# Optimization experiments

Hardware: AMD Instinct MI355X
Metric: run time of the kernel (lower is better)

The kernel has to match this reference:

```python
import jax, jax.numpy as jnp
import numpy as np

N, DEG, FIN, FOUT, K = 50000, 16, 32, 64, 3
E = N * DEG


def setup_inputs() -> dict:
    key = jax.random.key(0)
    ks = jax.random.split(key, 10)
    rng = np.random.default_rng(0)
    # unique edges sorted row-major (src*N+dst), ring guarantees deg_in/out>0
    ring = np.arange(N, dtype=np.int64) * N + (np.arange(N, dtype=np.int64) + 1) % N
    cand = np.unique(rng.integers(0, N * N, size=3 * E, dtype=np.int64))
    cand = np.setdiff1d(cand, ring, assume_unique=True)[: E - N]
    codes = np.sort(np.concatenate([cand, ring]))
    assert codes.shape[0] == E
    edge_index = jnp.asarray(np.stack([codes // N, codes % N]).astype(np.int32))
    X = jax.random.normal(ks[0], (N, FIN), jnp.float32)
    edge_weight = jax.random.uniform(ks[1], (E,), jnp.float32, 0.5, 1.5)
    cin = FIN + FOUT
    xav = float(np.sqrt(6.0 / (cin + FOUT)))
    def w(k):
        return jax.random.uniform(k, (2, K, cin, FOUT), jnp.float32, -xav, xav)
    return {
        'X': X, 'edge_index': edge_index, 'edge_weight': edge_weight,
        'Wz': w(ks[2]), 'bz': jnp.zeros((FOUT,), jnp.float32),
        'Wr': w(ks[3]), 'br': jnp.zeros((FOUT,), jnp.float32),
        'Wh': w(ks[4]), 'bh': jnp.zeros((FOUT,), jnp.float32),
    }


def _dconv(X, src, dst, rev_src, rev_dst, norm_out, norm_in, W, b):
    n = X.shape[0]
    def prop(x, s, d, nrm):  # out[d] += nrm * x[s]
        return jax.ops.segment_sum(nrm[:, None] * x[s], d, num_segments=n)
    H = X @ W[0, 0] + X @ W[1, 0]
    if W.shape[1] > 1:
        Tx1o = prop(X, src, dst, norm_out)
        Tx1i = prop(X, rev_src, rev_dst, norm_in)
        H = H + Tx1o @ W[0, 1] + Tx1i @ W[1, 1]
        for k in range(2, W.shape[1]):
            Tx1o = 2.0 * prop(Tx1o, src, dst, norm_out) - X
            Tx1i = 2.0 * prop(Tx1i, rev_src, rev_dst, norm_in) - X
            H = H + Tx1o @ W[0, k] + Tx1i @ W[1, k]
    return H + b


def reference(X, edge_index, edge_weight, Wz, bz, Wr, br, Wh, bh):
    n = X.shape[0]
    src, dst = edge_index[0], edge_index[1]
    deg_out = jax.ops.segment_sum(edge_weight, src, num_segments=n)
    deg_in = jax.ops.segment_sum(edge_weight, dst, num_segments=n)
    # faithful to original: both norms indexed by row (source)
    norm_out = 1.0 / deg_out[src]
    norm_in = 1.0 / deg_in[src]
    # reverse edges in dense_to_sparse(adj.T) order: sorted by (dst, src)
    order = jnp.argsort(dst.astype(jnp.int64) * n + src.astype(jnp.int64))
    rev_src, rev_dst = dst[order], src[order]
    H = jnp.zeros((n, Wz.shape[-1]), X.dtype)
    dc = lambda inp, W, b: _dconv(inp, src, dst, rev_src, rev_dst, norm_out, norm_in, W, b)
    Z = jax.nn.sigmoid(dc(jnp.concatenate([X, H], axis=1), Wz, bz))
    R = jax.nn.sigmoid(dc(jnp.concatenate([X, H], axis=1), Wr, br))
    H_tilde = jnp.tanh(dc(jnp.concatenate([X, H * R], axis=1), Wh, bh))
    return Z * H + (1.0 - Z) * H_tilde
```

## Files before the change

kernel.cpp:

```cpp
#include <hip/hip_runtime.h>
#include <hip/hip_fp16.h>
#include <cmath>

#define NN 50000
#define NE 800000
#define PADF 96
#define NBIN 391
#define NBLK 391
#define FCAP 3072
#define DST_HI 42949
#define SRC_CUT 33648

__device__ __forceinline__ unsigned short f2h(float f) {
  __half h = __float2half_rn(f);
  return *reinterpret_cast<unsigned short*>(&h);
}

typedef _Float16 half4 __attribute__((ext_vector_type(4)));
typedef float f32x4 __attribute__((ext_vector_type(4)));

__global__ __launch_bounds__(256) void k_aux(const float* __restrict__ X, const int* __restrict__ src,
                                             const int* __restrict__ dst, const float* __restrict__ ew,
                                             int* __restrict__ H,
                                             int* __restrict__ rptr, float* __restrict__ dout,
                                             const float* __restrict__ Wz, const float* __restrict__ Wh,
                                             unsigned short* __restrict__ WT, unsigned short* __restrict__ Xh,
                                             int* __restrict__ s0g) {
  __shared__ int hh[NBIN];
  __shared__ int s0l;
  int bid = blockIdx.x;
  int t = threadIdx.x;
  if (bid >= 667) {
    int h = bid - 667;
    hh[t] = 0;
    if (t + 256 < NBIN) hh[t + 256] = 0;
    if (t == 0) s0l = 0;
    __syncthreads();
    int my = 0;
#pragma unroll
    for (int r = 0; r < 8; ++r) {
      int e = h * 2048 + r * 256 + t;
      if (e < NE) {
        int d = dst[e];
        atomicAdd(&hh[d >> 7], 1);
        my += (d < DST_HI) ? 1 : 0;
        my += (d == DST_HI && src[e] < SRC_CUT) ? 1 : 0;
      }
    }
    atomicAdd(&s0l, my);
    __syncthreads();
    H[t * NBLK + h] = hh[t];
    if (t + 256 < NBIN) H[(t + 256) * NBLK + h] = hh[t + 256];
    if (t == 0) atomicAdd(s0g, s0l);
  } else if (bid < 196) {
    int i = bid * 256 + t;
    if (i >= NN) return;
    int lo = 0, hi = NE;
    while (lo < hi) { int m = (lo + hi) >> 1; if (src[m] < i) lo = m + 1; else hi = m; }
    int lo2 = lo, hi2 = NE;
    while (lo2 < hi2) { int m = (lo2 + hi2) >> 1; if (src[m] < i + 1) lo2 = m + 1; else hi2 = m; }
    rptr[i] = lo;
    if (i == NN - 1) rptr[NN] = lo2;
    float a = 0.f;
    for (int p = lo; p < lo2; ++p) a += ew[p];
    dout[i] = a;
  } else if (bid < 276) {
    int idx = (bid - 196) * 256 + t;
    int kk = idx >> 7, f = idx & 127;
    int blk = kk >> 5, c = kk & 31;
    const float* W = (f < 64) ? Wz : Wh;
    int fl = f & 63;
    float v;
    if (blk == 0)      v = W[c * 64 + fl] + W[18432 + c * 64 + fl];
    else if (blk == 1) v = W[6144 + c * 64 + fl];
    else if (blk == 2) v = W[18432 + 6144 + c * 64 + fl];
    else if (blk == 3) v = W[2 * 6144 + c * 64 + fl];
    else               v = W[18432 + 2 * 6144 + c * 64 + fl];
    WT[f * 160 + kk] = f2h(v);
  } else {
    int tt = (bid - 276) * 256 + t;
    int base = tt * 16;
    if (base >= NN * 32) return;
#pragma unroll
    for (int q = 0; q < 2; ++q) {
      const float4 a = *(const float4*)&X[base + q * 8];
      const float4 b = *(const float4*)&X[base + q * 8 + 4];
      ushort4 o1 = make_ushort4(f2h(a.x), f2h(a.y), f2h(a.z), f2h(a.w));
      ushort4 o2 = make_ushort4(f2h(b.x), f2h(b.y), f2h(b.z), f2h(b.w));
      *(ushort4*)&Xh[base + q * 8] = o1;
      *(ushort4*)&Xh[base + q * 8 + 4] = o2;
    }
  }
}

__global__ __launch_bounds__(512) void k_scanrow(int* __restrict__ H, int* __restrict__ rowtot) {
  __shared__ int tmp[512];
  int row = blockIdx.x;
  int t = threadIdx.x;
  int v = (t < NBLK) ? H[row * NBLK + t] : 0;
  tmp[t] = v;
  __syncthreads();
  for (int off = 1; off < 512; off <<= 1) {
    int u = (t >= (unsigned)off) ? tmp[t - off] : 0;
    __syncthreads();
    tmp[t] += u;
    __syncthreads();
  }
  if (t < NBLK) H[row * NBLK + t] = tmp[t] - v;
  if (t == 511) rowtot[row] = tmp[511];
}

__global__ __launch_bounds__(512) void k_part(const int* __restrict__ src, const int* __restrict__ dst,
                                              const int* __restrict__ P, const int* __restrict__ rowtot,
                                              unsigned long long* __restrict__ cmp64) {
  __shared__ int loc[NBIN];
  __shared__ int rs[512];
  __shared__ int rbase[NBIN];
  int h = blockIdx.x;
  int t = threadIdx.x;
  int v = (t < NBIN) ? rowtot[t] : 0;
  rs[t] = v;
  if (t < NBIN) loc[t] = 0;
  __syncthreads();
  for (int off = 1; off < 512; off <<= 1) {
    int u = (t >= (unsigned)off) ? rs[t - off] : 0;
    __syncthreads();
    rs[t] += u;
    __syncthreads();
  }
  if (t < NBIN) rbase[t] = rs[t] - v;
  __syncthreads();
#pragma unroll
  for (int r = 0; r < 4; ++r) {
    int e = h * 2048 + r * 512 + t;
    if (e < NE) {
      int d = dst[e];
      int bin = d >> 7;
      int rk = atomicAdd(&loc[bin], 1);
      int pos = rbase[bin] + P[bin * NBLK + h] + rk;
      cmp64[pos] = ((unsigned long long)(d & 127) << 48) |
                   ((unsigned long long)src[e] << 24) | (unsigned long long)e;
    }
  }
}

__global__ __launch_bounds__(512) void k_fine(const int* __restrict__ rowtot, const float* __restrict__ ew,
                                              const unsigned long long* __restrict__ cmp64,
                                              int2* __restrict__ cmp, int* __restrict__ sp,
                                              float* __restrict__ din) {
  __shared__ unsigned long long a1[FCAP], a2[FCAP];
  __shared__ int fh[128], fcnt[128], fo[129];
  __shared__ int bs[2];
  int cb = blockIdx.x;
  int t = threadIdx.x;
  if (t < 64) {
    int s = 0;
    for (int i = t; i < cb; i += 64) s += rowtot[i];
    s += __shfl_xor(s, 32, 64); s += __shfl_xor(s, 16, 64); s += __shfl_xor(s, 8, 64);
    s += __shfl_xor(s, 4, 64);  s += __shfl_xor(s, 2, 64);  s += __shfl_xor(s, 1, 64);
    if (t == 0) { bs[0] = s; bs[1] = s + rowtot[cb]; }
  }
  if (t < 128) { fh[t] = 0; fcnt[t] = 0; }
  __syncthreads();
  int base = bs[0];
  int m = bs[1] - base;
  if (m > FCAP) m = FCAP;
  for (int i = t; i < m; i += 512) {
    unsigned long long it = cmp64[base + i];
    a1[i] = it;
    atomicAdd(&fh[(int)(it >> 48)], 1);
  }
  __syncthreads();
  if (t < 64) {
    int v0 = fh[t * 2], v1 = fh[t * 2 + 1];
    int pair = v0 + v1;
    int run = pair;
    for (int off = 1; off < 64; off <<= 1) {
      int v = __shfl_up(run, off, 64);
      if (t >= off) run += v;
    }
    int excl = run - pair;
    fo[t * 2] = excl; fo[t * 2 + 1] = excl + v0;
    if (t == 63) fo[128] = excl + pair;
  }
  __syncthreads();
  for (int i = t; i < m; i += 512) {
    unsigned long long it = a1[i];
    int b = (int)(it >> 48);
    int p2 = fo[b] + atomicAdd(&fcnt[b], 1);
    a2[p2] = it;
  }
  if (t < 128) {
    int d = cb * 128 + t;
    if (d <= NN) sp[d] = base + fo[t];
  }
  __syncthreads();
  const int wv0 = t >> 6, lane = t & 63;
  for (int seg = wv0; seg < 128; seg += 8) {
    int d = cb * 128 + seg;
    if (d >= NN) break;
    int f0 = fo[seg], f1 = fo[seg + 1];
    int n = f1 - f0;
    int b0g = base + f0;
    if (n > 64) {
      if (lane == 0) {
        unsigned long long arr[PADF];
        int nn = n > PADF ? PADF : n;
        for (int i = 0; i < nn; ++i) arr[i] = a2[f0 + i];
        for (int i = 1; i < nn; ++i) {
          unsigned long long v = arr[i]; int j = i - 1;
          while (j >= 0 && arr[j] > v) { arr[j + 1] = arr[j]; --j; }
          arr[j + 1] = v;
        }
        float s = 0.f;
        for (int i = 0; i < nn; ++i) {
          unsigned long long it = arr[i];
          int e = (int)(it & 0xFFFFFF);
          int sc = (int)((it >> 24) & 0xFFFF);
          s += ew[e];
          cmp[b0g + i] = make_int2(e, (int)(((unsigned)d << 16) | (unsigned)sc));
        }
        din[d] = s;
      }
      continue;
    }
    unsigned long long k = ~0ULL;
    if (lane < n) k = a2[f0 + lane];
    if (n > 1) {
#pragma unroll
      for (int kk = 2; kk <= 64; kk <<= 1) {
#pragma unroll
        for (int j = kk >> 1; j > 0; j >>= 1) {
          unsigned long long o = __shfl_xor(k, j, 64);
          bool lower = (lane & j) == 0;
          bool asc = (lane & kk) == 0;
          bool keepmin = (lower == asc);
          if (keepmin ? (o < k) : (o > k)) k = o;
        }
      }
    }
    float wsum = 0.f;
    if (lane < n) {
      int e = (int)(k & 0xFFFFFF);
      int sc = (int)((k >> 24) & 0xFFFF);
      wsum = ew[e];
      cmp[b0g + lane] = make_int2(e, (int)(((unsigned)d << 16) | (unsigned)sc));
    }
    wsum += __shfl_xor(wsum, 32, 64); wsum += __shfl_xor(wsum, 16, 64);
    wsum += __shfl_xor(wsum, 8, 64);  wsum += __shfl_xor(wsum, 4, 64);
    wsum += __shfl_xor(wsum, 2, 64);  wsum += __shfl_xor(wsum, 1, 64);
    if (lane == 0) din[d] = wsum;
  }
}

__global__ __launch_bounds__(256) void k_emit(const int2* __restrict__ cmp, const int* __restrict__ rawsrc,
                                              const float* __restrict__ dout, const float* __restrict__ din,
                                              const int* __restrict__ s0g,
                                              int2* __restrict__ cnf, int2* __restrict__ cnr) {
  int i = blockIdx.x * 256 + threadIdx.x;
  if (i >= NE) return;
  int2 c = cmp[i];
  int e = c.x;
  unsigned y = (unsigned)c.y;
  int d = (int)(y >> 16), sc = (int)(y & 0xFFFF);
  cnf[i] = make_int2(sc, __float_as_int(1.0f / dout[sc]));
  int j = i - s0g[0]; if (j < 0) j += NE;
  cnr[e] = make_int2(d, __float_as_int(1.0f / din[rawsrc[j]]));
}

__global__ __launch_bounds__(256) void k_prop2(const unsigned short* __restrict__ inA, const int* __restrict__ rpA,
                                               const int2* __restrict__ cnA, unsigned short* __restrict__ outAh,
                                               const unsigned short* __restrict__ inB, const int* __restrict__ rpB,
                                               const int2* __restrict__ cnB, unsigned short* __restrict__ outBh,
                                               const float* __restrict__ sub, float mul) {
  int t = blockIdx.x * 256 + threadIdx.x;
  const int half = NN * 8;
  const unsigned short* in; const int* rp; const int2* cn; unsigned short* outh;
  if (t < half) { in = inA; rp = rpA; cn = cnA; outh = outAh; }
  else          { in = inB; rp = rpB; cn = cnB; outh = outBh; t -= half; }
  int r = t >> 3;
  if (r >= NN) return;
  int lane8 = t & 7;
  int c4 = lane8 * 4;
  int b = rp[r], e2 = rp[r + 1];
  float a0[4] = {0.f, 0.f, 0.f, 0.f}, a1[4] = {0.f, 0.f, 0.f, 0.f};
  int p = b;
#define GATH(cc, ww) { \
    uint2 bv = *(const uint2*)&in[(cc) * 32 + c4]; \
    float2 f01 = __half22float2(*(const __half2*)&bv.x); \
    float2 f23 = __half22float2(*(const __half2*)&bv.y); \
    float* a = (jj & 1) ? a1 : a0; \
    a[0] += (ww) * f01.x; a[1] += (ww) * f01.y; \
    a[2] += (ww) * f23.x; a[3] += (ww) * f23.y; }
  for (; p + 16 <= e2; p += 16) {
    int2 u = cn[p + lane8];
    int2 v = cn[p + 8 + lane8];
#pragma unroll
    for (int jj = 0; jj < 8; ++jj) {
      int col = __shfl(u.x, jj, 8);
      float w = __int_as_float(__shfl(u.y, jj, 8));
      GATH(col, w)
    }
#pragma unroll
    for (int jj = 0; jj < 8; ++jj) {
      int col = __shfl(v.x, jj, 8);
      float w = __int_as_float(__shfl(v.y, jj, 8));
      GATH(col, w)
    }
  }
  for (; p + 8 <= e2; p += 8) {
    int2 u = cn[p + lane8];
#pragma unroll
    for (int jj = 0; jj < 8; ++jj) {
      int col = __shfl(u.x, jj, 8);
      float w = __int_as_float(__shfl(u.y, jj, 8));
      GATH(col, w)
    }
  }
  for (int jj = 0; p < e2; ++p) {
    int2 c1 = cn[p];
    float w = __int_as_float(c1.y);
    GATH(c1.x, w)
  }
#undef GATH
  float ax = a0[0] + a1[0], ay = a0[1] + a1[1], az = a0[2] + a1[2], aw = a0[3] + a1[3];
  float4 o;
  if (sub) {
    const float4 s = *(const float4*)&sub[r * 32 + c4];
    o.x = mul * ax - s.x; o.y = mul * ay - s.y; o.z = mul * az - s.z; o.w = mul * aw - s.w;
  } else {
    o.x = ax; o.y = ay; o.z = az; o.w = aw;
  }
  ushort4 oh = make_ushort4(f2h(o.x), f2h(o.y), f2h(o.z), f2h(o.w));
  *(ushort4*)&outh[r * 32 + c4] = oh;
}

__global__ __launch_bounds__(256) void k_gemm(const unsigned short* __restrict__ Xh,
                                              const unsigned short* __restrict__ T1oh,
                                              const unsigned short* __restrict__ T1ih,
                                              const unsigned short* __restrict__ T2oh,
                                              const unsigned short* __restrict__ T2ih,
                                              const unsigned short* __restrict__ WT,
                                              const float* __restrict__ bz, const float* __restrict__ bh,
                                              float* __restrict__ out) {
  __shared__ unsigned short wlds[128 * 168];
  const int tid = threadIdx.x;
  for (int i = tid; i < 128 * 20; i += 256) {
    int n = i / 20, o = i % 20;
    *(uint4*)&wlds[n * 168 + o * 8] = *(const uint4*)&WT[n * 160 + o * 8];
  }
  __syncthreads();
  const int l = tid & 63, wid = tid >> 6;
  const int m0 = wid * 16;
  const int rb = blockIdx.x * 64;
  int grow = rb + m0 + (l & 15); if (grow >= NN) grow = NN - 1;
  const int kg = (l >> 4) * 4;
  f32x4 acc[8];
#pragma unroll
  for (int t = 0; t < 8; ++t) acc[t] = (f32x4){0.f, 0.f, 0.f, 0.f};
  const unsigned short* srcs[5] = {Xh, T1oh, T1ih, T2oh, T2ih};
#pragma unroll
  for (int s = 0; s < 5; ++s) {
    const unsigned short* A = srcs[s];
#pragma unroll
    for (int h2 = 0; h2 < 2; ++h2) {
      const int kk = h2 * 16;
      half4 af = *(const half4*)&A[grow * 32 + kk + kg];
      const int kglob = s * 32 + kk + kg;
#pragma unroll
      for (int t = 0; t < 8; ++t) {
        half4 bf = *(const half4*)&wlds[(t * 16 + (l & 15)) * 168 + kglob];
        acc[t] = __builtin_amdgcn_mfma_f32_16x16x16f16(af, bf, acc[t], 0, 0, 0);
      }
    }
  }
  const int c = l & 15;
#pragma unroll
  for (int t = 0; t < 4; ++t) {
    int col = t * 16 + c;
    float bzv = bz[col], bhv = bh[col];
#pragma unroll
    for (int i = 0; i < 4; ++i) {
      int r = rb + m0 + (l >> 4) * 4 + i;
      if (r < NN) {
        float z = 1.f / (1.f + expf(-(acc[t][i] + bzv)));
        float hv = tanhf(acc[t + 4][i] + bhv);
        out[r * 64 + col] = (1.f - z) * hv;
      }
    }
  }
}

extern "C" void kernel_launch(void* const* d_in, const int* in_sizes, int n_in,
                              void* d_out, int out_size, void* d_ws, size_t ws_size,
                              hipStream_t stream) {
  const float* X  = (const float*)d_in[0];
  const int*   ei = (const int*)d_in[1];
  const float* ew = (const float*)d_in[2];
  const float* Wz = (const float*)d_in[3];
  const float* bz = (const float*)d_in[4];
  const float* Wh = (const float*)d_in[7];
  const float* bh = (const float*)d_in[8];
  float* out = (float*)d_out;
  const int* src = ei;
  const int* dst = ei + NE;

  char* p = (char*)d_ws;
  auto alloc = [&](size_t bytes) -> char* {
    char* r = p;
    p += (bytes + 255) & ~(size_t)255;
    return r;
  };
  unsigned short* Xh   = (unsigned short*)alloc((size_t)NN * 32 * 2);
  unsigned short* T1oh = (unsigned short*)alloc((size_t)NN * 32 * 2);
  unsigned short* T1ih = (unsigned short*)alloc((size_t)NN * 32 * 2);
  unsigned short* T2oh = (unsigned short*)alloc((size_t)NN * 32 * 2);
  unsigned short* T2ih = (unsigned short*)alloc((size_t)NN * 32 * 2);
  unsigned long long* cmp64 = (unsigned long long*)alloc((size_t)NE * 8);
  int2*  cmp     = (int2*)alloc((size_t)NE * 8);
  int2*  cnf     = (int2*)alloc((size_t)NE * 8);
  int2*  cnr     = (int2*)alloc((size_t)NE * 8);
  int*   H       = (int*)alloc((size_t)NBIN * NBLK * 4);
  int*   rowtot  = (int*)alloc(NBIN * 4);
  int*   sp      = (int*)alloc((NN + 1) * 4);
  int*   rptr    = (int*)alloc((NN + 1) * 4);
  float* dout    = (float*)alloc(NN * 4);
  float* din     = (float*)alloc(NN * 4);
  unsigned short* WT = (unsigned short*)alloc(128 * 160 * 2);
  int*   s0g     = (int*)alloc(256);

  hipMemsetAsync(s0g, 0, 4, stream);
  k_aux<<<1058, 256, 0, stream>>>(X, src, dst, ew, H, rptr, dout, Wz, Wh, WT, Xh, s0g);
  k_scanrow<<<NBIN, 512, 0, stream>>>(H, rowtot);
  k_part<<<NBLK, 512, 0, stream>>>(src, dst, H, rowtot, cmp64);
  k_fine<<<NBIN, 512, 0, stream>>>(rowtot, ew, cmp64, cmp, sp, din);
  k_emit<<<3125, 256, 0, stream>>>(cmp, src, dout, din, s0g, cnf, cnr);

  k_prop2<<<3125, 256, 0, stream>>>(Xh, sp, cnf, T1oh,
                                    Xh, rptr, cnr, T1ih, nullptr, 1.f);
  k_prop2<<<3125, 256, 0, stream>>>(T1oh, sp, cnf, T2oh,
                                    T1ih, rptr, cnr, T2ih, X, 2.f);

  k_gemm<<<782, 256, 0, stream>>>(Xh, T1oh, T1ih, T2oh, T2ih, WT, bz, bh, out);
}
```

Baseline: 259.4 us.

## Move per-destination bitonic sort from k_fine into fused sort+emit kernel

The per-destination segment sort, previously done by 8 waves per block inside k_fine, moves into a new wave-per-node kernel (k_sortw). That kernel sorts each segment and writes the normalized forward and reverse edge arrays directly, replacing k_emit. k_fine now writes unsorted compacted entries and computes in-degree sums with 4 lanes per node. The aim is more parallelism for the sort across 12500 blocks. The cost is an extra read of cmp and scattered per-edge writes into cnr.

```diff
diff --git a/kernel.cpp b/kernel.cpp
--- a/kernel.cpp
+++ b/kernel.cpp
@@ -195,77 +195,80 @@
     if (d <= NN) sp[d] = base + fo[t];
   }
   __syncthreads();
-  const int wv0 = t >> 6, lane = t & 63;
-  for (int seg = wv0; seg < 128; seg += 8) {
-    int d = cb * 128 + seg;
-    if (d >= NN) break;
-    int f0 = fo[seg], f1 = fo[seg + 1];
-    int n = f1 - f0;
-    int b0g = base + f0;
-    if (n > 64) {
-      if (lane == 0) {
-        unsigned long long arr[PADF];
-        int nn = n > PADF ? PADF : n;
-        for (int i = 0; i < nn; ++i) arr[i] = a2[f0 + i];
-        for (int i = 1; i < nn; ++i) {
-          unsigned long long v = arr[i]; int j = i - 1;
-          while (j >= 0 && arr[j] > v) { arr[j + 1] = arr[j]; --j; }
-          arr[j + 1] = v;
-        }
-        float s = 0.f;
-        for (int i = 0; i < nn; ++i) {
-          unsigned long long it = arr[i];
-          int e = (int)(it & 0xFFFFFF);
-          int sc = (int)((it >> 24) & 0xFFFF);
-          s += ew[e];
-          cmp[b0g + i] = make_int2(e, (int)(((unsigned)d << 16) | (unsigned)sc));
-        }
-        din[d] = s;
-      }
-      continue;
-    }
-    unsigned long long k = ~0ULL;
-    if (lane < n) k = a2[f0 + lane];
-    if (n > 1) {
-#pragma unroll
-      for (int kk = 2; kk <= 64; kk <<= 1) {
-#pragma unroll
-        for (int j = kk >> 1; j > 0; j >>= 1) {
-          unsigned long long o = __shfl_xor(k, j, 64);
-          bool lower = (lane & j) == 0;
-          bool asc = (lane & kk) == 0;
-          bool keepmin = (lower == asc);
-          if (keepmin ? (o < k) : (o > k)) k = o;
-        }
-      }
-    }
-    float wsum = 0.f;
-    if (lane < n) {
-      int e = (int)(k & 0xFFFFFF);
-      int sc = (int)((k >> 24) & 0xFFFF);
-      wsum = ew[e];
-      cmp[b0g + lane] = make_int2(e, (int)(((unsigned)d << 16) | (unsigned)sc));
-    }
-    wsum += __shfl_xor(wsum, 32, 64); wsum += __shfl_xor(wsum, 16, 64);
-    wsum += __shfl_xor(wsum, 8, 64);  wsum += __shfl_xor(wsum, 4, 64);
-    wsum += __shfl_xor(wsum, 2, 64);  wsum += __shfl_xor(wsum, 1, 64);
-    if (lane == 0) din[d] = wsum;
-  }
-}
-
-__global__ __launch_bounds__(256) void k_emit(const int2* __restrict__ cmp, const int* __restrict__ rawsrc,
-                                              const float* __restrict__ dout, const float* __restrict__ din,
-                                              const int* __restrict__ s0g,
-                                              int2* __restrict__ cnf, int2* __restrict__ cnr) {
-  int i = blockIdx.x * 256 + threadIdx.x;
-  if (i >= NE) return;
-  int2 c = cmp[i];
-  int e = c.x;
-  unsigned y = (unsigned)c.y;
-  int d = (int)(y >> 16), sc = (int)(y & 0xFFFF);
-  cnf[i] = make_int2(sc, __float_as_int(1.0f / dout[sc]));
-  int j = i - s0g[0]; if (j < 0) j += NE;
-  cnr[e] = make_int2(d, __float_as_int(1.0f / din[rawsrc[j]]));
+  for (int i = t; i < m; i += 512) {
+    unsigned long long it = a2[i];
+    int e = (int)(it & 0xFFFFFF);
+    int sc = (int)((it >> 24) & 0xFFFF);
+    int d = cb * 128 + (int)(it >> 48);
+    cmp[base + i] = make_int2(e, (int)(((unsigned)d << 16) | (unsigned)sc));
+  }
+  int nd = t >> 2, ln = t & 3;
+  int d = cb * 128 + nd;
+  if (d < NN) {
+    float s = 0.f;
+    int e0 = fo[nd], e1 = fo[nd + 1];
+    for (int i = e0 + ln; i < e1; i += 4) s += ew[(int)(a2[i] & 0xFFFFFF)];
+    s += __shfl_down(s, 2, 4);
+    s += __shfl_down(s, 1, 4);
+    if (ln == 0) din[d] = s;
+  }
+}
+
+__global__ __launch_bounds__(256) void k_sortw(const int* __restrict__ sp, const int2* __restrict__ cmp,
+                                               const int* __restrict__ rawsrc,
+                                               const float* __restrict__ dout, const float* __restrict__ din,
+                                               const int* __restrict__ s0g,
+                                               int2* __restrict__ cnf, int2* __restrict__ cnr) {
+  int wv = (blockIdx.x * 256 + threadIdx.x) >> 6;
+  int lane = threadIdx.x & 63;
+  if (wv >= NN) return;
+  int b0 = sp[wv], b1 = sp[wv + 1];
+  int n = b1 - b0;
+  int s0 = s0g[0];
+  if (n > 64) {
+    if (lane == 0) {
+      int es[PADF]; unsigned ys[PADF];
+      int nn = n > PADF ? PADF : n;
+      for (int i = 0; i < nn; ++i) { int2 pe = cmp[b0 + i]; es[i] = pe.x; ys[i] = (unsigned)pe.y; }
+      for (int i = 1; i < nn; ++i) {
+        int ve = es[i]; unsigned vy = ys[i]; int j = i - 1;
+        while (j >= 0 && ys[j] > vy) { es[j + 1] = es[j]; ys[j + 1] = ys[j]; --j; }
+        es[j + 1] = ve; ys[j + 1] = vy;
+      }
+      for (int i = 0; i < nn; ++i) {
+        int sc = (int)(ys[i] & 0xFFFF);
+        cnf[b0 + i] = make_int2(sc, __float_as_int(1.0f / dout[sc]));
+        int j = b0 + i - s0; if (j < 0) j += NE;
+        cnr[es[i]] = make_int2(wv, __float_as_int(1.0f / din[rawsrc[j]]));
+      }
+    }
+    return;
+  }
+  unsigned long long k = ~0ULL;
+  if (lane < n) {
+    int2 pe = cmp[b0 + lane];
+    k = ((unsigned long long)(unsigned)pe.y << 32) | (unsigned)pe.x;
+  }
+  if (n > 1) {
+#pragma unroll
+    for (int kk = 2; kk <= 64; kk <<= 1) {
+#pragma unroll
+      for (int j = kk >> 1; j > 0; j >>= 1) {
+        unsigned long long o = __shfl_xor(k, j, 64);
+        bool lower = (lane & j) == 0;
+        bool asc = (lane & kk) == 0;
+        bool keepmin = (lower == asc);
+        if (keepmin ? (o < k) : (o > k)) k = o;
+      }
+    }
+  }
+  if (lane < n) {
+    int e = (int)(k & 0xffffffffu);
+    int sc = (int)((k >> 32) & 0xFFFF);
+    cnf[b0 + lane] = make_int2(sc, __float_as_int(1.0f / dout[sc]));
+    int j = b0 + lane - s0; if (j < 0) j += NE;
+    cnr[e] = make_int2(wv, __float_as_int(1.0f / din[rawsrc[j]]));
+  }
 }
 
 __global__ __launch_bounds__(256) void k_prop2(const unsigned short* __restrict__ inA, const int* __restrict__ rpA,
@@ -434,7 +437,7 @@
   k_scanrow<<<NBIN, 512, 0, stream>>>(H, rowtot);
   k_part<<<NBLK, 512, 0, stream>>>(src, dst, H, rowtot, cmp64);
   k_fine<<<NBIN, 512, 0, stream>>>(rowtot, ew, cmp64, cmp, sp, din);
-  k_emit<<<3125, 256, 0, stream>>>(cmp, src, dout, din, s0g, cnf, cnr);
+  k_sortw<<<12500, 256, 0, stream>>>(sp, cmp, src, dout, din, s0g, cnf, cnr);
 
   k_prop2<<<3125, 256, 0, stream>>>(Xh, sp, cnf, T1oh,
                                     Xh, rptr, cnr, T1ih, nullptr, 1.f);
```

Result: faster. 233.5 us (-10.0%).
